# Optimization experiments

Measured on AMD Instinct MI355X. Metric: run time of the kernel, lower is better.

The kernel has to match this reference:

```python
import jax, jax.numpy as jnp
import numpy as np

D = 512; N = 4096; NH = 16; DEPTH = 3; MLP = 4; GENES = 250; GH = 64; GW = 64


def setup_inputs() -> dict:
    key = jax.random.key(0)
    ks = jax.random.split(key, 10)
    gf = jax.random.normal(ks[0], (N, D), jnp.float32)
    # unique spot positions: permutation of the 64x64 grid cells
    perm = jax.random.permutation(ks[1], GH * GW)[:N]
    coords = jnp.stack([perm // GW, perm % GW], axis=1).astype(jnp.int32)
    s = 0.02
    rn = lambda k, sh: jax.random.normal(k, sh, jnp.float32) * s
    return dict(
        global_feats=gf, coords=coords, grid_h=GH, grid_w=GW,
        ln1_g=jnp.ones((DEPTH, D)), ln1_b=jnp.zeros((DEPTH, D)),
        wqkv=rn(ks[2], (DEPTH, 3 * D, D)), bqkv=jnp.zeros((DEPTH, 3 * D)),
        wo=rn(ks[3], (DEPTH, D, D)), bo=jnp.zeros((DEPTH, D)),
        ln2_g=jnp.ones((DEPTH, D)), ln2_b=jnp.zeros((DEPTH, D)),
        w1=rn(ks[4], (DEPTH, MLP * D, D)), b1=jnp.zeros((DEPTH, MLP * D)),
        w2=rn(ks[5], (DEPTH, D, MLP * D)), b2=jnp.zeros((DEPTH, D)),
        ck=rn(ks[6], (DEPTH, D, 1, 3, 3)), cb=jnp.zeros((DEPTH, D)),
        lnf_g=jnp.ones((D,)), lnf_b=jnp.zeros((D,)),
        wp=rn(ks[7], (GENES, D)), bp=jnp.zeros((GENES,)),
    )


def _ln(x, g, b, eps=1e-5):
    m = jnp.mean(x, axis=-1, keepdims=True)
    v = jnp.var(x, axis=-1, keepdims=True)
    return (x - m) * jax.lax.rsqrt(v + eps) * g + b


def reference(global_feats, coords, grid_h, grid_w, ln1_g, ln1_b, wqkv, bqkv,
              wo, bo, ln2_g, ln2_b, w1, b1, w2, b2, ck, cb, lnf_g, lnf_b, wp, bp):
    x = global_feats  # [N, D]
    n, d = x.shape
    nh = NH; dh = d // nh
    rows = coords[:, 0]; cols = coords[:, 1]
    for i in range(ln1_g.shape[0]):
        # --- self-attention (eval mode, dropout off) ---
        xn = _ln(x, ln1_g[i], ln1_b[i])
        qkv = xn @ wqkv[i].T + bqkv[i]                      # [N, 3D]
        q, k, v = jnp.split(qkv, 3, axis=-1)
        q = q.reshape(n, nh, dh).transpose(1, 0, 2)        # [H, N, dh]
        k = k.reshape(n, nh, dh).transpose(1, 0, 2)
        v = v.reshape(n, nh, dh).transpose(1, 0, 2)
        att = jax.nn.softmax(jnp.einsum('hqd,hkd->hqk', q, k) * (dh ** -0.5), axis=-1)
        ao = jnp.einsum('hqk,hkd->hqd', att, v).transpose(1, 0, 2).reshape(n, d)
        x = x + (ao @ wo[i].T + bo[i])
        # --- MLP ---
        h = jax.nn.gelu(_ln(x, ln2_g[i], ln2_b[i]) @ w1[i].T + b1[i], approximate=False)
        x = x + (h @ w2[i].T + b2[i])
        # --- APEG: scatter -> depthwise conv -> gather ---
        grid = jnp.zeros((d, grid_h, grid_w), x.dtype).at[:, rows, cols].set(x.T)
        co = jax.lax.conv_general_dilated(
            grid[None], ck[i], window_strides=(1, 1), padding=((1, 1), (1, 1)),
            dimension_numbers=('NCHW', 'OIHW', 'NCHW'), feature_group_count=d)[0]
        co = co + cb[i][:, None, None]
        x = x + co[:, rows, cols].T
    x = _ln(x, lnf_g, lnf_b)
    pred = x @ wp.T + bp
    return (x, pred)
```

## Files before the change

### kernel.cpp

```cpp
#include <hip/hip_runtime.h>
#include <math.h>

#define D 512
#define N_TOK 4096
#define NHEAD 16
#define DH 32
#define DEPTH 3
#define MLPD 2048
#define GENES 250
#define GH 64
#define GW 64

typedef __attribute__((ext_vector_type(8))) short short8;
typedef __attribute__((ext_vector_type(4))) float f32x4;
typedef unsigned short ushort_t;

#define AS1 __attribute__((address_space(1)))
#define AS3 __attribute__((address_space(3)))

#if defined(__has_builtin)
#if __has_builtin(__builtin_amdgcn_exp2f)
#define EXP2F(x) __builtin_amdgcn_exp2f(x)
#endif
#endif
#ifndef EXP2F
#define EXP2F(x) __expf(0.69314718056f * (x))
#endif

__device__ __forceinline__ unsigned short f2bf(float f) {
  unsigned int u = __float_as_uint(f);
  u += 0x7fffu + ((u >> 16) & 1u);
  return (unsigned short)(u >> 16);
}
__device__ __forceinline__ unsigned int bfpack(float a, float b) {
  return __builtin_amdgcn_perm(__float_as_uint(b), __float_as_uint(a), 0x07060302u);
}
__device__ __forceinline__ void gload_lds16(const ushort_t* g, ushort_t* l) {
  __builtin_amdgcn_global_load_lds(
      (const AS1 unsigned int*)g,
      (AS3 unsigned int*)(unsigned int)(unsigned long long)l, 16, 0, 0);
}
__device__ __forceinline__ int perm64(int m) {
  int mi = m >> 4, g = (m >> 2) & 3, r = m & 3;
  return ((mi & 1) << 5) | (g << 3) | ((mi >> 1) << 2) | r;
}

__global__ __launch_bounds__(256) void ln_kernel(const float* __restrict__ x,
    const float* __restrict__ g, const float* __restrict__ b,
    float* __restrict__ yf, ushort_t* __restrict__ ybf,
    float* __restrict__ xcopy) {
  int row = blockIdx.x;
  int t = threadIdx.x;
  const float* xr = x + (size_t)row * D;
  float v0 = xr[t], v1 = xr[t + 256];
  if (xcopy) {
    xcopy[(size_t)row * D + t] = v0;
    xcopy[(size_t)row * D + t + 256] = v1;
  }
  float s = v0 + v1;
  float sq = v0 * v0 + v1 * v1;
#pragma unroll
  for (int off = 32; off > 0; off >>= 1) {
    s += __shfl_down(s, off, 64);
    sq += __shfl_down(sq, off, 64);
  }
  __shared__ float s1[4], s2[4];
  int wid = t >> 6, lane = t & 63;
  if (lane == 0) { s1[wid] = s; s2[wid] = sq; }
  __syncthreads();
  float tot = s1[0] + s1[1] + s1[2] + s1[3];
  float totq = s2[0] + s2[1] + s2[2] + s2[3];
  float mean = tot * (1.0f / D);
  float var = totq * (1.0f / D) - mean * mean;
  float rs = rsqrtf(var + 1e-5f);
  float r0 = (v0 - mean) * rs * g[t] + b[t];
  float r1 = (v1 - mean) * rs * g[t + 256] + b[t + 256];
  if (yf) { yf[(size_t)row * D + t] = r0; yf[(size_t)row * D + t + 256] = r1; }
  if (ybf) {
    ybf[(size_t)row * D + t] = f2bf(r0);
    ybf[(size_t)row * D + t + 256] = f2bf(r1);
  }
}

template <int TM, int TN, int NKH>
__global__ __launch_bounds__(256) void gemm_bf(
    const ushort_t* __restrict__ A, const ushort_t* __restrict__ B,
    const float* __restrict__ bias, const float* __restrict__ res,
    float* __restrict__ C, ushort_t* __restrict__ Cbf,
    ushort_t* __restrict__ qO, ushort_t* __restrict__ kO, ushort_t* __restrict__ vO,
    int K, int ldc, int nstore, int mode) {
  constexpr int MI = TM / 32;
  constexpr int NI = TN / 32;
  __shared__ ushort_t As[2][NKH][TM * 32];
  __shared__ ushort_t Bs[2][NKH][TN * 32];
  int t = threadIdx.x;
  int w = t >> 6, lane = t & 63;
  int g = lane >> 4, c = lane & 15;
  int orig = blockIdx.y * gridDim.x + blockIdx.x;
  int cpx = (gridDim.x * gridDim.y) >> 3;
  int wid2 = (orig & 7) * cpx + (orig >> 3);
  int bn = (wid2 % gridDim.x) * TN;
  int bm = (wid2 / gridDim.x) * TM;
  int wr = (w >> 1) * (TM / 2);
  int wc = (w & 1) * (TN / 2);

  const ushort_t* gA = A + (size_t)(bm + (t >> 2)) * K + (t & 3) * 8;
  const ushort_t* gB = B + (size_t)(bn + (t >> 2)) * K + (t & 3) * 8;

  auto stage = [&](int p, int koff) {
#pragma unroll
    for (int h = 0; h < NKH; ++h) {
      gload_lds16(gA + koff + h * 32, &As[p][h][t * 8]);
      if (TM == 128)
        gload_lds16(gA + koff + h * 32 + (size_t)64 * K, &As[p][h][(t + 256) * 8]);
      gload_lds16(gB + koff + h * 32, &Bs[p][h][t * 8]);
      if (TN == 128)
        gload_lds16(gB + koff + h * 32 + (size_t)64 * K, &Bs[p][h][(t + 256) * 8]);
    }
  };

  f32x4 acc[MI][NI] = {};

  const int niter = K / (32 * NKH);
  stage(0, 0);
  __syncthreads();
  for (int it = 0; it < niter; ++it) {
    int p = it & 1;
    if (it + 1 < niter) stage(p ^ 1, (it + 1) * 32 * NKH);
#pragma unroll
    for (int kh = 0; kh < NKH; ++kh) {
      short8 af[MI], bfr[NI];
#pragma unroll
      for (int mi = 0; mi < MI; ++mi)
        af[mi] = *(const short8*)&As[p][kh][(wr + mi * 16 + c) * 32 + g * 8];
#pragma unroll
      for (int ni = 0; ni < NI; ++ni)
        bfr[ni] = *(const short8*)&Bs[p][kh][(wc + ni * 16 + c) * 32 + g * 8];
#pragma unroll
      for (int mi = 0; mi < MI; ++mi)
#pragma unroll
        for (int ni = 0; ni < NI; ++ni)
          acc[mi][ni] = __builtin_amdgcn_mfma_f32_16x16x32_bf16(
              af[mi], bfr[ni], acc[mi][ni], 0, 0, 0);
    }
    __syncthreads();
  }

  const float qs_scale = 0.17677669529663688f * 1.4426950408889634f;
  if (mode == 2) {
#pragma unroll
    for (int ni = 0; ni < NI; ++ni) {
      int col = bn + wc + ni * 16 + c;
      float bv = bias[col];
      int which = col >> 9;
      int h = (col >> 5) & 15;
      int d = col & 31;
      size_t hb = (size_t)h * (N_TOK * DH);
#pragma unroll
      for (int mi = 0; mi < MI; ++mi) {
        int row0 = bm + wr + mi * 16 + g * 4;
        float v0 = acc[mi][ni][0] + bv;
        float v1 = acc[mi][ni][1] + bv;
        float v2 = acc[mi][ni][2] + bv;
        float v3 = acc[mi][ni][3] + bv;
        if (which == 0) {
          qO[hb + (size_t)(row0 + 0) * DH + d] = f2bf(v0 * qs_scale);
          qO[hb + (size_t)(row0 + 1) * DH + d] = f2bf(v1 * qs_scale);
          qO[hb + (size_t)(row0 + 2) * DH + d] = f2bf(v2 * qs_scale);
          qO[hb + (size_t)(row0 + 3) * DH + d] = f2bf(v3 * qs_scale);
        } else if (which == 1) {
          kO[hb + (size_t)(row0 + 0) * DH + d] = f2bf(v0);
          kO[hb + (size_t)(row0 + 1) * DH + d] = f2bf(v1);
          kO[hb + (size_t)(row0 + 2) * DH + d] = f2bf(v2);
          kO[hb + (size_t)(row0 + 3) * DH + d] = f2bf(v3);
        } else {
          int m = row0 & 63;
          int mi_l = m >> 4, g_l = (m >> 2) & 3;
          int nb = ((mi_l & 1) << 5) | (g_l << 3) | ((mi_l >> 1) << 2);
          uint2 pk;
          pk.x = (unsigned)f2bf(v0) | ((unsigned)f2bf(v1) << 16);
          pk.y = (unsigned)f2bf(v2) | ((unsigned)f2bf(v3) << 16);
          *(uint2*)(vO + hb + (size_t)d * N_TOK + (row0 & ~63) + nb) = pk;
        }
      }
    }
    return;
  }
#pragma unroll
  for (int ni = 0; ni < NI; ++ni) {
    int col = bn + wc + ni * 16 + c;
    float bv = bias[col];
    bool cok = col < nstore;
#pragma unroll
    for (int mi = 0; mi < MI; ++mi) {
      int row0 = bm + wr + mi * 16 + g * 4;
#pragma unroll
      for (int reg = 0; reg < 4; ++reg) {
        int row = row0 + reg;
        float v = acc[mi][ni][reg] + bv;
        if (mode == 0) {
          size_t idx = (size_t)row * ldc + col;
          if (cok) {
            if (res) v += res[idx];
            C[idx] = v;
          }
        } else {
          v = 0.5f * v * (1.0f + erff(v * 0.70710678118654752f));
          Cbf[(size_t)row * ldc + col] = f2bf(v);
        }
      }
    }
  }
}

#define KST 40
#define VTST 72

__global__ __launch_bounds__(256) void attn_mfma(
    const ushort_t* __restrict__ qb, const ushort_t* __restrict__ kb,
    const ushort_t* __restrict__ vtb, ushort_t* __restrict__ ao) {
  __shared__ ushort_t Ks[64 * KST];
  __shared__ ushort_t Vts[32 * VTST];
  int qt = blockIdx.x, head = blockIdx.y;
  int t = threadIdx.x;
  int w = t >> 6, lane = t & 63;
  int g = lane >> 4, c = lane & 15;
  const size_t hbase = (size_t)head * (N_TOK * DH);
  int q0 = qt * 128 + w * 32;

  short8 qf[2];
  qf[0] = *(const short8*)(qb + hbase + (size_t)(q0 + c) * DH + g * 8);
  qf[1] = *(const short8*)(qb + hbase + (size_t)(q0 + 16 + c) * DH + g * 8);

  short8 ones;
#pragma unroll
  for (int i = 0; i < 8; ++i) ones[i] = (short)0x3F80;

  f32x4 o[2][2] = {};
  f32x4 lf[2] = {};
  const f32x4 zf = {0.f, 0.f, 0.f, 0.f};

  const ushort_t* kg = kb + hbase + (size_t)(t >> 2) * DH + (t & 3) * 8;
  const ushort_t* vg = vtb + hbase + (size_t)(t >> 3) * N_TOK + (t & 7) * 8;
  ushort_t* kw = &Ks[(t >> 2) * KST + (t & 3) * 8];
  ushort_t* vw = &Vts[(t >> 3) * VTST + (t & 7) * 8];

  short8 kreg = *(const short8*)kg;
  short8 vreg = *(const short8*)vg;

  typedef union { short8 s8; unsigned int u32[4]; } pk_t;

  for (int tile = 0; tile < N_TOK / 64; ++tile) {
    __syncthreads();
    *(short8*)kw = kreg;
    *(short8*)vw = vreg;
    __syncthreads();
    if (tile + 1 < N_TOK / 64) {
      kreg = *(const short8*)(kg + (size_t)(tile + 1) * 64 * DH);
      vreg = *(const short8*)(vg + (tile + 1) * 64);
    }

    short8 kf[4];
#pragma unroll
    for (int mi = 0; mi < 4; ++mi)
      kf[mi] = *(const short8*)&Ks[(mi * 16 + c) * KST + g * 8];
    short8 vf[2][2];
#pragma unroll
    for (int half = 0; half < 2; ++half)
#pragma unroll
      for (int ch = 0; ch < 2; ++ch)
        vf[half][ch] = *(const short8*)&Vts[(half * 16 + c) * VTST + ch * 32 + g * 8];

    short8 pf[2][2];
#pragma unroll
    for (int qs = 0; qs < 2; ++qs) {
      f32x4 sp[4];
#pragma unroll
      for (int mi = 0; mi < 4; ++mi)
        sp[mi] = __builtin_amdgcn_mfma_f32_16x16x32_bf16(kf[mi], qf[qs], zf, 0, 0, 0);
      float pr[4][4];
#pragma unroll
      for (int mi = 0; mi < 4; ++mi)
#pragma unroll
        for (int r = 0; r < 4; ++r) pr[mi][r] = EXP2F(sp[mi][r]);
      pk_t p0, p1;
      p0.u32[0] = bfpack(pr[0][0], pr[0][1]);
      p0.u32[1] = bfpack(pr[0][2], pr[0][3]);
      p0.u32[2] = bfpack(pr[2][0], pr[2][1]);
      p0.u32[3] = bfpack(pr[2][2], pr[2][3]);
      p1.u32[0] = bfpack(pr[1][0], pr[1][1]);
      p1.u32[1] = bfpack(pr[1][2], pr[1][3]);
      p1.u32[2] = bfpack(pr[3][0], pr[3][1]);
      p1.u32[3] = bfpack(pr[3][2], pr[3][3]);
      pf[qs][0] = p0.s8;
      pf[qs][1] = p1.s8;
    }

#pragma unroll
    for (int qs = 0; qs < 2; ++qs) {
#pragma unroll
      for (int ch = 0; ch < 2; ++ch) {
        lf[qs] = __builtin_amdgcn_mfma_f32_16x16x32_bf16(ones, pf[qs][ch], lf[qs], 0, 0, 0);
#pragma unroll
        for (int half = 0; half < 2; ++half)
          o[qs][half] = __builtin_amdgcn_mfma_f32_16x16x32_bf16(
              vf[half][ch], pf[qs][ch], o[qs][half], 0, 0, 0);
      }
    }
  }

#pragma unroll
  for (int qs = 0; qs < 2; ++qs) {
    float inv = 1.0f / lf[qs][0];
    int q = q0 + qs * 16 + c;
    ushort_t* op = ao + (size_t)q * D + head * DH;
#pragma unroll
    for (int half = 0; half < 2; ++half)
#pragma unroll
      for (int reg = 0; reg < 4; ++reg)
        op[half * 16 + g * 4 + reg] = f2bf(o[qs][half][reg] * inv);
  }
}

__global__ void scatter_kernel(const int* __restrict__ coords,
                               int* __restrict__ pos2tok) {
  int n = blockIdx.x * 256 + threadIdx.x;
  if (n < N_TOK) pos2tok[coords[2 * n] * GW + coords[2 * n + 1]] = n;
}

__global__ __launch_bounds__(256) void conv_ln_kernel(
    const float* __restrict__ xin, float* __restrict__ xout,
    const float* __restrict__ ck, const float* __restrict__ cb,
    const int* __restrict__ pos2tok, const int* __restrict__ coords,
    const float* __restrict__ g, const float* __restrict__ b,
    float* __restrict__ yf, ushort_t* __restrict__ ybf) {
  int n = blockIdx.x, t = threadIdx.x;
  __shared__ int nb[9];
  if (t < 9) {
    int r = coords[2 * n], c = coords[2 * n + 1];
    int dy = t / 3 - 1, dx = t % 3 - 1;
    int rr = r + dy, cc = c + dx;
    nb[t] = (rr >= 0 && rr < GH && cc >= 0 && cc < GW) ? pos2tok[rr * GW + cc] : -1;
  }
  __syncthreads();
  float v[2];
#pragma unroll
  for (int j = 0; j < 2; ++j) {
    int ch = t + j * 256;
    float s = cb[ch];
#pragma unroll
    for (int tap = 0; tap < 9; ++tap) {
      int tok = nb[tap];
      if (tok >= 0) s = fmaf(ck[ch * 9 + tap], xin[(size_t)tok * D + ch], s);
    }
    v[j] = xin[(size_t)n * D + ch] + s;
    xout[(size_t)n * D + ch] = v[j];
  }
  float s = v[0] + v[1];
  float sq = v[0] * v[0] + v[1] * v[1];
#pragma unroll
  for (int off = 32; off > 0; off >>= 1) {
    s += __shfl_down(s, off, 64);
    sq += __shfl_down(sq, off, 64);
  }
  __shared__ float s1[4], s2[4];
  int wid = t >> 6, lane = t & 63;
  if (lane == 0) { s1[wid] = s; s2[wid] = sq; }
  __syncthreads();
  float tot = s1[0] + s1[1] + s1[2] + s1[3];
  float totq = s2[0] + s2[1] + s2[2] + s2[3];
  float mean = tot * (1.0f / D);
  float var = totq * (1.0f / D) - mean * mean;
  float rs = rsqrtf(var + 1e-5f);
  float r0 = (v[0] - mean) * rs * g[t] + b[t];
  float r1 = (v[1] - mean) * rs * g[t + 256] + b[t + 256];
  if (yf) { yf[(size_t)n * D + t] = r0; yf[(size_t)n * D + t + 256] = r1; }
  ybf[(size_t)n * D + t] = f2bf(r0);
  ybf[(size_t)n * D + t + 256] = f2bf(r1);
}

#define CS0 (DEPTH * 3 * D * D)
#define CS1 (DEPTH * D * D)
#define CS2 (DEPTH * MLPD * D)
#define CS3 (DEPTH * D * MLPD)
#define CS4 (256 * D)
#define CT0 (CS0)
#define CT1 (CT0 + CS1)
#define CT2 (CT1 + CS2)
#define CT3 (CT2 + CS3)
#define CT4 (CT3 + CS4)
#define NB_CAST (CT4 / 4 / 256)

__global__ __launch_bounds__(256) void castw_all(
    const float* __restrict__ wqkv, const float* __restrict__ wo,
    const float* __restrict__ w1, const float* __restrict__ w2,
    const float* __restrict__ wp, const float* __restrict__ bp,
    ushort_t* __restrict__ dst, float* __restrict__ bp_pad) {
  if (blockIdx.x == NB_CAST) {
    int i = threadIdx.x;
    bp_pad[i] = (i < GENES) ? bp[i] : 0.f;
    return;
  }
  int i = (blockIdx.x * 256 + threadIdx.x) * 4;
  const float* src;
  int si, ns;
  if (i < CT0)      { src = wqkv; si = i;       ns = CS0; }
  else if (i < CT1) { src = wo;   si = i - CT0; ns = CS1; }
  else if (i < CT2) { src = w1;   si = i - CT1; ns = CS2; }
  else if (i < CT3) { src = w2;   si = i - CT2; ns = CS3; }
  else              { src = wp;   si = i - CT3; ns = GENES * D; }
  unsigned long long pk = 0;
#pragma unroll
  for (int j = 0; j < 4; ++j) {
    float v = (si + j < ns) ? src[si + j] : 0.f;
    pk |= ((unsigned long long)f2bf(v)) << (16 * j);
  }
  *(unsigned long long*)(dst + i) = pk;
}

extern "C" void kernel_launch(void* const* d_in, const int* in_sizes, int n_in,
                              void* d_out, int out_size, void* d_ws, size_t ws_size,
                              hipStream_t stream) {
  const float* gf     = (const float*)d_in[0];
  const int*   coords = (const int*)d_in[1];
  const float* ln1_g  = (const float*)d_in[4];
  const float* ln1_b  = (const float*)d_in[5];
  const float* wqkv   = (const float*)d_in[6];
  const float* bqkv   = (const float*)d_in[7];
  const float* wo     = (const float*)d_in[8];
  const float* bo     = (const float*)d_in[9];
  const float* ln2_g  = (const float*)d_in[10];
  const float* ln2_b  = (const float*)d_in[11];
  const float* w1     = (const float*)d_in[12];
  const float* b1     = (const float*)d_in[13];
  const float* w2     = (const float*)d_in[14];
  const float* b2     = (const float*)d_in[15];
  const float* ck     = (const float*)d_in[16];
  const float* cb     = (const float*)d_in[17];
  const float* lnf_g  = (const float*)d_in[18];
  const float* lnf_b  = (const float*)d_in[19];
  const float* wp     = (const float*)d_in[20];
  const float* bp     = (const float*)d_in[21];
  float* out = (float*)d_out;

  const size_t ND = (size_t)N_TOK * D;
  float* xb0 = (float*)d_ws;
  float* xb1 = xb0 + ND;
  ushort_t* xn_bf  = (ushort_t*)(xb1 + ND);
  ushort_t* ao_bf  = xn_bf + ND;
  ushort_t* out_bf = ao_bf + ND;
  ushort_t* shared = out_bf + ND;
  ushort_t* qb   = shared;
  ushort_t* kbuf = qb + ND;
  ushort_t* vtb  = kbuf + ND;
  ushort_t* h_bf = shared;
  ushort_t* wqkv_bf = shared + (size_t)N_TOK * MLPD;
  ushort_t* wo_bf = wqkv_bf + DEPTH * 3 * D * D;
  ushort_t* w1_bf = wo_bf + DEPTH * D * D;
  ushort_t* w2_bf = w1_bf + DEPTH * MLPD * D;
  ushort_t* wp_bf = w2_bf + DEPTH * D * MLPD;
  float* bp_pad = (float*)(wp_bf + 256 * D);
  int* pos2tok = (int*)(bp_pad + 256);

  scatter_kernel<<<(N_TOK + 255) / 256, 256, 0, stream>>>(coords, pos2tok);

  castw_all<<<NB_CAST + 1, 256, 0, stream>>>(
      wqkv, wo, w1, w2, wp, bp, wqkv_bf, bp_pad);

  ln_kernel<<<N_TOK, 256, 0, stream>>>(gf, ln1_g, ln1_b, nullptr, xn_bf, xb0);

  float* x  = xb0;
  float* xo = xb1;
  for (int i = 0; i < DEPTH; ++i) {
    gemm_bf<128, 64, 2><<<dim3(24, 32), 256, 0, stream>>>(
        xn_bf, wqkv_bf + (size_t)i * 3 * D * D, bqkv + (size_t)i * 3 * D,
        nullptr, nullptr, nullptr, qb, kbuf, vtb, D, 0, 3 * D, 2);
    attn_mfma<<<dim3(N_TOK / 128, NHEAD), 256, 0, stream>>>(qb, kbuf, vtb, ao_bf);
    gemm_bf<64, 64, 2><<<dim3(8, 64), 256, 0, stream>>>(
        ao_bf, wo_bf + (size_t)i * D * D, bo + (size_t)i * D,
        x, x, nullptr, nullptr, nullptr, nullptr, D, D, D, 0);
    ln_kernel<<<N_TOK, 256, 0, stream>>>(x, ln2_g + i * D, ln2_b + i * D,
                                         nullptr, xn_bf, nullptr);
    gemm_bf<128, 128, 2><<<dim3(16, 32), 256, 0, stream>>>(
        xn_bf, w1_bf + (size_t)i * MLPD * D, b1 + (size_t)i * MLPD,
        nullptr, nullptr, h_bf, nullptr, nullptr, nullptr, D, MLPD, MLPD, 1);
    gemm_bf<64, 64, 4><<<dim3(8, 64), 256, 0, stream>>>(
        h_bf, w2_bf + (size_t)i * D * MLPD, b2 + (size_t)i * D,
        x, x, nullptr, nullptr, nullptr, nullptr, MLPD, D, D, 0);
    if (i < DEPTH - 1) {
      conv_ln_kernel<<<N_TOK, 256, 0, stream>>>(
          x, xo, ck + (size_t)i * D * 9, cb + (size_t)i * D, pos2tok, coords,
          ln1_g + (i + 1) * D, ln1_b + (i + 1) * D, nullptr, xn_bf);
    } else {
      conv_ln_kernel<<<N_TOK, 256, 0, stream>>>(
          x, xo, ck + (size_t)i * D * 9, cb + (size_t)i * D, pos2tok, coords,
          lnf_g, lnf_b, out, out_bf);
    }
    float* tmp = x; x = xo; xo = tmp;
  }
  gemm_bf<64, 64, 2><<<dim3(4, 64), 256, 0, stream>>>(
      out_bf, wp_bf, bp_pad, nullptr, out + ND, nullptr, nullptr, nullptr, nullptr,
      D, GENES, GENES, 0);
}
```

Measured before the change: 579.1 us.

## Fuse output-projection and MLP-down GEMMs with following LN/conv via cooperative grid sync

Merges the Wo GEMM with the following LayerNorm, and the MLP second GEMM with the APEG conv+LN, into single cooperative kernels that use a grid-wide sync between the GEMM epilogue and a per-row phase. The three setup kernels (scatter, weight cast, first LN) are also combined into one launch. The goal is to remove kernel launch gaps and tail effects between dependent stages. In exchange, it relies on all 512 blocks being co-resident for the grid sync, and the MLP-down GEMM drops from NKH=4 to NKH=2.

Measured after the change: 1.461 ms. 2.52x slower.

```diff
diff --git a/kernel.cpp b/kernel.cpp
--- a/kernel.cpp
+++ b/kernel.cpp
@@ -1,5 +1,8 @@
 #include <hip/hip_runtime.h>
+#include <hip/hip_cooperative_groups.h>
 #include <math.h>
+
+namespace cg = cooperative_groups;
 
 #define D 512
 #define N_TOK 4096
@@ -40,31 +43,86 @@
       (const AS1 unsigned int*)g,
       (AS3 unsigned int*)(unsigned int)(unsigned long long)l, 16, 0, 0);
 }
-__device__ __forceinline__ int perm64(int m) {
-  int mi = m >> 4, g = (m >> 2) & 3, r = m & 3;
-  return ((mi & 1) << 5) | (g << 3) | ((mi >> 1) << 2) | r;
-}
-
-__global__ __launch_bounds__(256) void ln_kernel(const float* __restrict__ x,
+
+template <int TM, int TN, int NKH>
+__device__ __forceinline__ void gemm_tile(
+    const ushort_t* __restrict__ A, const ushort_t* __restrict__ B,
+    int K, int& bm_o, int& bn_o, f32x4 (&acc)[TM / 32][TN / 32]) {
+  constexpr int MI = TM / 32;
+  constexpr int NI = TN / 32;
+  __shared__ ushort_t As[2][NKH][TM * 32];
+  __shared__ ushort_t Bs[2][NKH][TN * 32];
+  int t = threadIdx.x;
+  int w = t >> 6, lane = t & 63;
+  int gq = lane >> 4, c = lane & 15;
+  int orig = blockIdx.y * gridDim.x + blockIdx.x;
+  int cpx = (gridDim.x * gridDim.y) >> 3;
+  int wid2 = (orig & 7) * cpx + (orig >> 3);
+  int bn = (wid2 % gridDim.x) * TN;
+  int bm = (wid2 / gridDim.x) * TM;
+  bm_o = bm;
+  bn_o = bn;
+  int wr = (w >> 1) * (TM / 2);
+  int wc = (w & 1) * (TN / 2);
+
+  const ushort_t* gA = A + (size_t)(bm + (t >> 2)) * K + (t & 3) * 8;
+  const ushort_t* gB = B + (size_t)(bn + (t >> 2)) * K + (t & 3) * 8;
+
+  auto stage = [&](int p, int koff) {
+#pragma unroll
+    for (int h = 0; h < NKH; ++h) {
+      gload_lds16(gA + koff + h * 32, &As[p][h][t * 8]);
+      if (TM == 128)
+        gload_lds16(gA + koff + h * 32 + (size_t)64 * K, &As[p][h][(t + 256) * 8]);
+      gload_lds16(gB + koff + h * 32, &Bs[p][h][t * 8]);
+      if (TN == 128)
+        gload_lds16(gB + koff + h * 32 + (size_t)64 * K, &Bs[p][h][(t + 256) * 8]);
+    }
+  };
+
+#pragma unroll
+  for (int mi = 0; mi < MI; ++mi)
+#pragma unroll
+    for (int ni = 0; ni < NI; ++ni) acc[mi][ni] = (f32x4){0.f, 0.f, 0.f, 0.f};
+
+  const int niter = K / (32 * NKH);
+  stage(0, 0);
+  __syncthreads();
+  for (int it = 0; it < niter; ++it) {
+    int p = it & 1;
+    if (it + 1 < niter) stage(p ^ 1, (it + 1) * 32 * NKH);
+#pragma unroll
+    for (int kh = 0; kh < NKH; ++kh) {
+      short8 af[MI], bfr[NI];
+#pragma unroll
+      for (int mi = 0; mi < MI; ++mi)
+        af[mi] = *(const short8*)&As[p][kh][(wr + mi * 16 + c) * 32 + gq * 8];
+#pragma unroll
+      for (int ni = 0; ni < NI; ++ni)
+        bfr[ni] = *(const short8*)&Bs[p][kh][(wc + ni * 16 + c) * 32 + gq * 8];
+#pragma unroll
+      for (int mi = 0; mi < MI; ++mi)
+#pragma unroll
+        for (int ni = 0; ni < NI; ++ni)
+          acc[mi][ni] = __builtin_amdgcn_mfma_f32_16x16x32_bf16(
+              af[mi], bfr[ni], acc[mi][ni], 0, 0, 0);
+    }
+    __syncthreads();
+  }
+}
+
+__device__ __forceinline__ void ln_row_body(const float* __restrict__ xr,
     const float* __restrict__ g, const float* __restrict__ b,
-    float* __restrict__ yf, ushort_t* __restrict__ ybf,
-    float* __restrict__ xcopy) {
-  int row = blockIdx.x;
+    float* __restrict__ yfr, ushort_t* __restrict__ ybfr,
+    float* s1, float* s2) {
   int t = threadIdx.x;
-  const float* xr = x + (size_t)row * D;
   float v0 = xr[t], v1 = xr[t + 256];
-  if (xcopy) {
-    xcopy[(size_t)row * D + t] = v0;
-    xcopy[(size_t)row * D + t + 256] = v1;
-  }
-  float s = v0 + v1;
-  float sq = v0 * v0 + v1 * v1;
+  float s = v0 + v1, sq = v0 * v0 + v1 * v1;
 #pragma unroll
   for (int off = 32; off > 0; off >>= 1) {
     s += __shfl_down(s, off, 64);
     sq += __shfl_down(sq, off, 64);
   }
-  __shared__ float s1[4], s2[4];
   int wid = t >> 6, lane = t & 63;
   if (lane == 0) { s1[wid] = s; s2[wid] = sq; }
   __syncthreads();
@@ -75,11 +133,10 @@
   float rs = rsqrtf(var + 1e-5f);
   float r0 = (v0 - mean) * rs * g[t] + b[t];
   float r1 = (v1 - mean) * rs * g[t + 256] + b[t + 256];
-  if (yf) { yf[(size_t)row * D + t] = r0; yf[(size_t)row * D + t + 256] = r1; }
-  if (ybf) {
-    ybf[(size_t)row * D + t] = f2bf(r0);
-    ybf[(size_t)row * D + t + 256] = f2bf(r1);
-  }
+  if (yfr) { yfr[t] = r0; yfr[t + 256] = r1; }
+  ybfr[t] = f2bf(r0);
+  ybfr[t + 256] = f2bf(r1);
+  __syncthreads();
 }
 
 template <int TM, int TN, int NKH>
@@ -91,60 +148,14 @@
     int K, int ldc, int nstore, int mode) {
   constexpr int MI = TM / 32;
   constexpr int NI = TN / 32;
-  __shared__ ushort_t As[2][NKH][TM * 32];
-  __shared__ ushort_t Bs[2][NKH][TN * 32];
+  f32x4 acc[MI][NI];
+  int bm, bn;
+  gemm_tile<TM, TN, NKH>(A, B, K, bm, bn, acc);
   int t = threadIdx.x;
   int w = t >> 6, lane = t & 63;
   int g = lane >> 4, c = lane & 15;
-  int orig = blockIdx.y * gridDim.x + blockIdx.x;
-  int cpx = (gridDim.x * gridDim.y) >> 3;
-  int wid2 = (orig & 7) * cpx + (orig >> 3);
-  int bn = (wid2 % gridDim.x) * TN;
-  int bm = (wid2 / gridDim.x) * TM;
   int wr = (w >> 1) * (TM / 2);
   int wc = (w & 1) * (TN / 2);
-
-  const ushort_t* gA = A + (size_t)(bm + (t >> 2)) * K + (t & 3) * 8;
-  const ushort_t* gB = B + (size_t)(bn + (t >> 2)) * K + (t & 3) * 8;
-
-  auto stage = [&](int p, int koff) {
-#pragma unroll
-    for (int h = 0; h < NKH; ++h) {
-      gload_lds16(gA + koff + h * 32, &As[p][h][t * 8]);
-      if (TM == 128)
-        gload_lds16(gA + koff + h * 32 + (size_t)64 * K, &As[p][h][(t + 256) * 8]);
-      gload_lds16(gB + koff + h * 32, &Bs[p][h][t * 8]);
-      if (TN == 128)
-        gload_lds16(gB + koff + h * 32 + (size_t)64 * K, &Bs[p][h][(t + 256) * 8]);
-    }
-  };
-
-  f32x4 acc[MI][NI] = {};
-
-  const int niter = K / (32 * NKH);
-  stage(0, 0);
-  __syncthreads();
-  for (int it = 0; it < niter; ++it) {
-    int p = it & 1;
-    if (it + 1 < niter) stage(p ^ 1, (it + 1) * 32 * NKH);
-#pragma unroll
-    for (int kh = 0; kh < NKH; ++kh) {
-      short8 af[MI], bfr[NI];
-#pragma unroll
-      for (int mi = 0; mi < MI; ++mi)
-        af[mi] = *(const short8*)&As[p][kh][(wr + mi * 16 + c) * 32 + g * 8];
-#pragma unroll
-      for (int ni = 0; ni < NI; ++ni)
-        bfr[ni] = *(const short8*)&Bs[p][kh][(wc + ni * 16 + c) * 32 + g * 8];
-#pragma unroll
-      for (int mi = 0; mi < MI; ++mi)
-#pragma unroll
-        for (int ni = 0; ni < NI; ++ni)
-          acc[mi][ni] = __builtin_amdgcn_mfma_f32_16x16x32_bf16(
-              af[mi], bfr[ni], acc[mi][ni], 0, 0, 0);
-    }
-    __syncthreads();
-  }
 
   const float qs_scale = 0.17677669529663688f * 1.4426950408889634f;
   if (mode == 2) {
@@ -213,6 +224,125 @@
   }
 }
 
+__global__ __launch_bounds__(256) void wo_ln_fused(
+    const ushort_t* __restrict__ A, const ushort_t* __restrict__ B,
+    const float* __restrict__ bias, float* __restrict__ x,
+    const float* __restrict__ lg, const float* __restrict__ lb,
+    ushort_t* __restrict__ ybf) {
+  f32x4 acc[2][2];
+  int bm, bn;
+  gemm_tile<64, 64, 2>(A, B, D, bm, bn, acc);
+  int t = threadIdx.x;
+  int w = t >> 6, lane = t & 63;
+  int gq = lane >> 4, c = lane & 15;
+  int wr = (w >> 1) * 32, wc = (w & 1) * 32;
+#pragma unroll
+  for (int ni = 0; ni < 2; ++ni) {
+    int col = bn + wc + ni * 16 + c;
+    float bv = bias[col];
+#pragma unroll
+    for (int mi = 0; mi < 2; ++mi) {
+      int row0 = bm + wr + mi * 16 + gq * 4;
+#pragma unroll
+      for (int reg = 0; reg < 4; ++reg) {
+        size_t idx = (size_t)(row0 + reg) * D + col;
+        x[idx] = acc[mi][ni][reg] + bv + x[idx];
+      }
+    }
+  }
+  __threadfence();
+  cg::this_grid().sync();
+  __shared__ float s1[4], s2[4];
+  int bid = blockIdx.y * gridDim.x + blockIdx.x;
+#pragma unroll 1
+  for (int r = 0; r < 8; ++r) {
+    int row = bid * 8 + r;
+    ln_row_body(x + (size_t)row * D, lg, lb, nullptr,
+                ybf + (size_t)row * D, s1, s2);
+  }
+}
+
+__global__ __launch_bounds__(256) void mlp2_convln_fused(
+    const ushort_t* __restrict__ A, const ushort_t* __restrict__ B,
+    const float* __restrict__ bias, float* __restrict__ x,
+    float* __restrict__ xout, const float* __restrict__ ck,
+    const float* __restrict__ cb, const int* __restrict__ pos2tok,
+    const int* __restrict__ coords, const float* __restrict__ lg,
+    const float* __restrict__ lb, float* __restrict__ yf,
+    ushort_t* __restrict__ ybf) {
+  f32x4 acc[2][2];
+  int bm, bn;
+  gemm_tile<64, 64, 2>(A, B, MLPD, bm, bn, acc);
+  int t = threadIdx.x;
+  int w = t >> 6, lane = t & 63;
+  int gq = lane >> 4, c = lane & 15;
+  int wr = (w >> 1) * 32, wc = (w & 1) * 32;
+#pragma unroll
+  for (int ni = 0; ni < 2; ++ni) {
+    int col = bn + wc + ni * 16 + c;
+    float bv = bias[col];
+#pragma unroll
+    for (int mi = 0; mi < 2; ++mi) {
+      int row0 = bm + wr + mi * 16 + gq * 4;
+#pragma unroll
+      for (int reg = 0; reg < 4; ++reg) {
+        size_t idx = (size_t)(row0 + reg) * D + col;
+        x[idx] = acc[mi][ni][reg] + bv + x[idx];
+      }
+    }
+  }
+  __threadfence();
+  cg::this_grid().sync();
+  __shared__ int nb[9];
+  __shared__ float s1[4], s2[4];
+  int bid = blockIdx.y * gridDim.x + blockIdx.x;
+#pragma unroll 1
+  for (int r8 = 0; r8 < 8; ++r8) {
+    int n = bid * 8 + r8;
+    if (t < 9) {
+      int rr0 = coords[2 * n], cc0 = coords[2 * n + 1];
+      int dy = t / 3 - 1, dx = t % 3 - 1;
+      int rr = rr0 + dy, cc = cc0 + dx;
+      nb[t] = (rr >= 0 && rr < GH && cc >= 0 && cc < GW) ? pos2tok[rr * GW + cc] : -1;
+    }
+    __syncthreads();
+    float v[2];
+#pragma unroll
+    for (int j = 0; j < 2; ++j) {
+      int ch = t + j * 256;
+      float s = cb[ch];
+#pragma unroll
+      for (int tap = 0; tap < 9; ++tap) {
+        int tok = nb[tap];
+        if (tok >= 0) s = fmaf(ck[ch * 9 + tap], x[(size_t)tok * D + ch], s);
+      }
+      v[j] = x[(size_t)n * D + ch] + s;
+      xout[(size_t)n * D + ch] = v[j];
+    }
+    float s = v[0] + v[1];
+    float sq = v[0] * v[0] + v[1] * v[1];
+#pragma unroll
+    for (int off = 32; off > 0; off >>= 1) {
+      s += __shfl_down(s, off, 64);
+      sq += __shfl_down(sq, off, 64);
+    }
+    int wid = t >> 6;
+    if (lane == 0) { s1[wid] = s; s2[wid] = sq; }
+    __syncthreads();
+    float tot = s1[0] + s1[1] + s1[2] + s1[3];
+    float totq = s2[0] + s2[1] + s2[2] + s2[3];
+    float mean = tot * (1.0f / D);
+    float var = totq * (1.0f / D) - mean * mean;
+    float rs = rsqrtf(var + 1e-5f);
+    float r0 = (v[0] - mean) * rs * lg[t] + lb[t];
+    float r1 = (v[1] - mean) * rs * lg[t + 256] + lb[t + 256];
+    if (yf) { yf[(size_t)n * D + t] = r0; yf[(size_t)n * D + t + 256] = r1; }
+    ybf[(size_t)n * D + t] = f2bf(r0);
+    ybf[(size_t)n * D + t + 256] = f2bf(r1);
+    __syncthreads();
+  }
+}
+
 #define KST 40
 #define VTST 72
 
@@ -322,63 +452,6 @@
   }
 }
 
-__global__ void scatter_kernel(const int* __restrict__ coords,
-                               int* __restrict__ pos2tok) {
-  int n = blockIdx.x * 256 + threadIdx.x;
-  if (n < N_TOK) pos2tok[coords[2 * n] * GW + coords[2 * n + 1]] = n;
-}
-
-__global__ __launch_bounds__(256) void conv_ln_kernel(
-    const float* __restrict__ xin, float* __restrict__ xout,
-    const float* __restrict__ ck, const float* __restrict__ cb,
-    const int* __restrict__ pos2tok, const int* __restrict__ coords,
-    const float* __restrict__ g, const float* __restrict__ b,
-    float* __restrict__ yf, ushort_t* __restrict__ ybf) {
-  int n = blockIdx.x, t = threadIdx.x;
-  __shared__ int nb[9];
-  if (t < 9) {
-    int r = coords[2 * n], c = coords[2 * n + 1];
-    int dy = t / 3 - 1, dx = t % 3 - 1;
-    int rr = r + dy, cc = c + dx;
-    nb[t] = (rr >= 0 && rr < GH && cc >= 0 && cc < GW) ? pos2tok[rr * GW + cc] : -1;
-  }
-  __syncthreads();
-  float v[2];
-#pragma unroll
-  for (int j = 0; j < 2; ++j) {
-    int ch = t + j * 256;
-    float s = cb[ch];
-#pragma unroll
-    for (int tap = 0; tap < 9; ++tap) {
-      int tok = nb[tap];
-      if (tok >= 0) s = fmaf(ck[ch * 9 + tap], xin[(size_t)tok * D + ch], s);
-    }
-    v[j] = xin[(size_t)n * D + ch] + s;
-    xout[(size_t)n * D + ch] = v[j];
-  }
-  float s = v[0] + v[1];
-  float sq = v[0] * v[0] + v[1] * v[1];
-#pragma unroll
-  for (int off = 32; off > 0; off >>= 1) {
-    s += __shfl_down(s, off, 64);
-    sq += __shfl_down(sq, off, 64);
-  }
-  __shared__ float s1[4], s2[4];
-  int wid = t >> 6, lane = t & 63;
-  if (lane == 0) { s1[wid] = s; s2[wid] = sq; }
-  __syncthreads();
-  float tot = s1[0] + s1[1] + s1[2] + s1[3];
-  float totq = s2[0] + s2[1] + s2[2] + s2[3];
-  float mean = tot * (1.0f / D);
-  float var = totq * (1.0f / D) - mean * mean;
-  float rs = rsqrtf(var + 1e-5f);
-  float r0 = (v[0] - mean) * rs * g[t] + b[t];
-  float r1 = (v[1] - mean) * rs * g[t + 256] + b[t + 256];
-  if (yf) { yf[(size_t)n * D + t] = r0; yf[(size_t)n * D + t + 256] = r1; }
-  ybf[(size_t)n * D + t] = f2bf(r0);
-  ybf[(size_t)n * D + t + 256] = f2bf(r1);
-}
-
 #define CS0 (DEPTH * 3 * D * D)
 #define CS1 (DEPTH * D * D)
 #define CS2 (DEPTH * MLPD * D)
@@ -390,32 +463,72 @@
 #define CT3 (CT2 + CS3)
 #define CT4 (CT3 + CS4)
 #define NB_CAST (CT4 / 4 / 256)
-
-__global__ __launch_bounds__(256) void castw_all(
+#define SC_BLKS 16
+#define SETUP_BLKS (SC_BLKS + NB_CAST + 1 + N_TOK)
+
+__global__ __launch_bounds__(256) void setup_all(
+    const int* __restrict__ coords, int* __restrict__ pos2tok,
     const float* __restrict__ wqkv, const float* __restrict__ wo,
     const float* __restrict__ w1, const float* __restrict__ w2,
     const float* __restrict__ wp, const float* __restrict__ bp,
-    ushort_t* __restrict__ dst, float* __restrict__ bp_pad) {
-  if (blockIdx.x == NB_CAST) {
-    int i = threadIdx.x;
-    bp_pad[i] = (i < GENES) ? bp[i] : 0.f;
+    ushort_t* __restrict__ wdst, float* __restrict__ bp_pad,
+    const float* __restrict__ gf, const float* __restrict__ ln1_g,
+    const float* __restrict__ ln1_b, float* __restrict__ xb0,
+    ushort_t* __restrict__ xn_bf) {
+  int bx = blockIdx.x;
+  int t = threadIdx.x;
+  if (bx < SC_BLKS) {
+    int n = bx * 256 + t;
+    if (n < N_TOK) pos2tok[coords[2 * n] * GW + coords[2 * n + 1]] = n;
     return;
   }
-  int i = (blockIdx.x * 256 + threadIdx.x) * 4;
-  const float* src;
-  int si, ns;
-  if (i < CT0)      { src = wqkv; si = i;       ns = CS0; }
-  else if (i < CT1) { src = wo;   si = i - CT0; ns = CS1; }
-  else if (i < CT2) { src = w1;   si = i - CT1; ns = CS2; }
-  else if (i < CT3) { src = w2;   si = i - CT2; ns = CS3; }
-  else              { src = wp;   si = i - CT3; ns = GENES * D; }
-  unsigned long long pk = 0;
-#pragma unroll
-  for (int j = 0; j < 4; ++j) {
-    float v = (si + j < ns) ? src[si + j] : 0.f;
-    pk |= ((unsigned long long)f2bf(v)) << (16 * j);
-  }
-  *(unsigned long long*)(dst + i) = pk;
+  if (bx < SC_BLKS + NB_CAST + 1) {
+    int cb_ = bx - SC_BLKS;
+    if (cb_ == NB_CAST) {
+      bp_pad[t] = (t < GENES) ? bp[t] : 0.f;
+      return;
+    }
+    int i = (cb_ * 256 + t) * 4;
+    const float* src;
+    int si, ns;
+    if (i < CT0)      { src = wqkv; si = i;       ns = CS0; }
+    else if (i < CT1) { src = wo;   si = i - CT0; ns = CS1; }
+    else if (i < CT2) { src = w1;   si = i - CT1; ns = CS2; }
+    else if (i < CT3) { src = w2;   si = i - CT2; ns = CS3; }
+    else              { src = wp;   si = i - CT3; ns = GENES * D; }
+    unsigned long long pk = 0;
+#pragma unroll
+    for (int j = 0; j < 4; ++j) {
+      float v = (si + j < ns) ? src[si + j] : 0.f;
+      pk |= ((unsigned long long)f2bf(v)) << (16 * j);
+    }
+    *(unsigned long long*)(wdst + i) = pk;
+    return;
+  }
+  int row = bx - (SC_BLKS + NB_CAST + 1);
+  const float* xr = gf + (size_t)row * D;
+  float v0 = xr[t], v1 = xr[t + 256];
+  xb0[(size_t)row * D + t] = v0;
+  xb0[(size_t)row * D + t + 256] = v1;
+  float s = v0 + v1, sq = v0 * v0 + v1 * v1;
+#pragma unroll
+  for (int off = 32; off > 0; off >>= 1) {
+    s += __shfl_down(s, off, 64);
+    sq += __shfl_down(sq, off, 64);
+  }
+  __shared__ float s1[4], s2[4];
+  int wid = t >> 6, lane = t & 63;
+  if (lane == 0) { s1[wid] = s; s2[wid] = sq; }
+  __syncthreads();
+  float tot = s1[0] + s1[1] + s1[2] + s1[3];
+  float totq = s2[0] + s2[1] + s2[2] + s2[3];
+  float mean = tot * (1.0f / D);
+  float var = totq * (1.0f / D) - mean * mean;
+  float rs = rsqrtf(var + 1e-5f);
+  float r0 = (v0 - mean) * rs * ln1_g[t] + ln1_b[t];
+  float r1 = (v1 - mean) * rs * ln1_g[t + 256] + ln1_b[t + 256];
+  xn_bf[(size_t)row * D + t] = f2bf(r0);
+  xn_bf[(size_t)row * D + t + 256] = f2bf(r1);
 }
 
 extern "C" void kernel_launch(void* const* d_in, const int* in_sizes, int n_in,
@@ -462,12 +575,9 @@
   float* bp_pad = (float*)(wp_bf + 256 * D);
   int* pos2tok = (int*)(bp_pad + 256);
 
-  scatter_kernel<<<(N_TOK + 255) / 256, 256, 0, stream>>>(coords, pos2tok);
-
-  castw_all<<<NB_CAST + 1, 256, 0, stream>>>(
-      wqkv, wo, w1, w2, wp, bp, wqkv_bf, bp_pad);
-
-  ln_kernel<<<N_TOK, 256, 0, stream>>>(gf, ln1_g, ln1_b, nullptr, xn_bf, xb0);
+  setup_all<<<SETUP_BLKS, 256, 0, stream>>>(
+      coords, pos2tok, wqkv, wo, w1, w2, wp, bp, wqkv_bf, bp_pad,
+      gf, ln1_g, ln1_b, xb0, xn_bf);
 
   float* x  = xb0;
   float* xo = xb1;
@@ -476,25 +586,39 @@
         xn_bf, wqkv_bf + (size_t)i * 3 * D * D, bqkv + (size_t)i * 3 * D,
         nullptr, nullptr, nullptr, qb, kbuf, vtb, D, 0, 3 * D, 2);
     attn_mfma<<<dim3(N_TOK / 128, NHEAD), 256, 0, stream>>>(qb, kbuf, vtb, ao_bf);
-    gemm_bf<64, 64, 2><<<dim3(8, 64), 256, 0, stream>>>(
-        ao_bf, wo_bf + (size_t)i * D * D, bo + (size_t)i * D,
-        x, x, nullptr, nullptr, nullptr, nullptr, D, D, D, 0);
-    ln_kernel<<<N_TOK, 256, 0, stream>>>(x, ln2_g + i * D, ln2_b + i * D,
-                                         nullptr, xn_bf, nullptr);
+    {
+      const ushort_t* Ap = ao_bf;
+      const ushort_t* Bp = wo_bf + (size_t)i * D * D;
+      const float* biasp = bo + (size_t)i * D;
+      float* xp = x;
+      const float* lgp = ln2_g + (size_t)i * D;
+      const float* lbp = ln2_b + (size_t)i * D;
+      ushort_t* ybfp = xn_bf;
+      void* args[] = {&Ap, &Bp, &biasp, &xp, &lgp, &lbp, &ybfp};
+      hipLaunchCooperativeKernel((const void*)wo_ln_fused, dim3(8, 64),
+                                 dim3(256), args, 0, stream);
+    }
     gemm_bf<128, 128, 2><<<dim3(16, 32), 256, 0, stream>>>(
         xn_bf, w1_bf + (size_t)i * MLPD * D, b1 + (size_t)i * MLPD,
         nullptr, nullptr, h_bf, nullptr, nullptr, nullptr, D, MLPD, MLPD, 1);
-    gemm_bf<64, 64, 4><<<dim3(8, 64), 256, 0, stream>>>(
-        h_bf, w2_bf + (size_t)i * D * MLPD, b2 + (size_t)i * D,
-        x, x, nullptr, nullptr, nullptr, nullptr, MLPD, D, D, 0);
-    if (i < DEPTH - 1) {
-      conv_ln_kernel<<<N_TOK, 256, 0, stream>>>(
-          x, xo, ck + (size_t)i * D * 9, cb + (size_t)i * D, pos2tok, coords,
-          ln1_g + (i + 1) * D, ln1_b + (i + 1) * D, nullptr, xn_bf);
-    } else {
-      conv_ln_kernel<<<N_TOK, 256, 0, stream>>>(
-          x, xo, ck + (size_t)i * D * 9, cb + (size_t)i * D, pos2tok, coords,
-          lnf_g, lnf_b, out, out_bf);
+    {
+      const ushort_t* Ap = h_bf;
+      const ushort_t* Bp = w2_bf + (size_t)i * D * MLPD;
+      const float* biasp = b2 + (size_t)i * D;
+      float* xp = x;
+      float* xop = xo;
+      const float* ckp = ck + (size_t)i * D * 9;
+      const float* cbp = cb + (size_t)i * D;
+      const int* p2tp = pos2tok;
+      const int* cop = coords;
+      const float* lgp = (i < DEPTH - 1) ? ln1_g + (size_t)(i + 1) * D : lnf_g;
+      const float* lbp = (i < DEPTH - 1) ? ln1_b + (size_t)(i + 1) * D : lnf_b;
+      float* yfp = (i < DEPTH - 1) ? nullptr : out;
+      ushort_t* ybfp = (i < DEPTH - 1) ? xn_bf : out_bf;
+      void* args[] = {&Ap, &Bp, &biasp, &xp, &xop, &ckp, &cbp,
+                      &p2tp, &cop, &lgp, &lbp, &yfp, &ybfp};
+      hipLaunchCooperativeKernel((const void*)mlp2_convln_fused, dim3(8, 64),
+                                 dim3(256), args, 0, stream);
     }
     float* tmp = x; x = xo; xo = tmp;
   }
```
